# Kernel optimization log

Hardware: AMD Instinct MI355X
Metric: run time of the kernel (lower is better)

## Reference

```python
import jax, jax.numpy as jnp
import numpy as np

D_MODEL = 1024
N_HEADS = 16
HEAD_DIM = D_MODEL // N_HEADS
D_FF = 4096
LN_EPS = 1e-5


def _layernorm(x, g, b):
    mu = jnp.mean(x, axis=-1, keepdims=True)
    var = jnp.var(x, axis=-1, keepdims=True)
    return (x - mu) * jax.lax.rsqrt(var + LN_EPS) * g + b


def setup_inputs() -> dict:
    key = jax.random.key(0)
    ks = jax.random.split(key, 10)
    s = 0.02
    return {
        "hidden_states": jax.random.normal(ks[0], (2, 2048, D_MODEL), dtype=jnp.float32),
        "qkv_w": jax.random.normal(ks[1], (3 * D_MODEL, D_MODEL), dtype=jnp.float32) * s,
        "qkv_b": jnp.zeros((3 * D_MODEL,), dtype=jnp.float32),
        "out_w": jax.random.normal(ks[2], (D_MODEL, D_MODEL), dtype=jnp.float32) * s,
        "out_b": jnp.zeros((D_MODEL,), dtype=jnp.float32),
        "fc1_w": jax.random.normal(ks[3], (D_FF, D_MODEL), dtype=jnp.float32) * s,
        "fc1_b": jnp.zeros((D_FF,), dtype=jnp.float32),
        "fc2_w": jax.random.normal(ks[4], (D_MODEL, D_FF), dtype=jnp.float32) * s,
        "fc2_b": jnp.zeros((D_MODEL,), dtype=jnp.float32),
        "ln1_g": jnp.ones((D_MODEL,), dtype=jnp.float32),
        "ln1_b": jnp.zeros((D_MODEL,), dtype=jnp.float32),
        "ln2_g": jnp.ones((D_MODEL,), dtype=jnp.float32),
        "ln2_b": jnp.zeros((D_MODEL,), dtype=jnp.float32),
    }


def reference(hidden_states, qkv_w, qkv_b, out_w, out_b, fc1_w, fc1_b, fc2_w, fc2_b, ln1_g, ln1_b, ln2_g, ln2_b):
    B, S, D = hidden_states.shape
    scale = 1.0 / np.sqrt(HEAD_DIM).astype(np.float32)

    normed = _layernorm(hidden_states, ln1_g, ln1_b)
    qkv = normed @ qkv_w.T + qkv_b  # [B,S,3D]
    qkv = qkv.reshape(B, S, 3, N_HEADS, HEAD_DIM).transpose(2, 0, 3, 1, 4)
    q, k, v = qkv[0], qkv[1], qkv[2]  # [B,H,S,hd]

    scores = jnp.einsum("bhqd,bhkd->bhqk", q, k) * scale
    causal = jnp.tril(jnp.ones((S, S), dtype=bool))
    scores = jnp.where(causal, scores, jnp.float32(-jnp.inf))
    probs = jax.nn.softmax(scores, axis=-1)
    attn = jnp.einsum("bhqk,bhkd->bhqd", probs, v)  # [B,H,S,hd]
    attn = attn.transpose(0, 2, 1, 3).reshape(B, S, D)
    attn = attn @ out_w.T + out_b

    hidden = hidden_states + attn
    normed2 = _layernorm(hidden, ln2_g, ln2_b)
    ff = jax.nn.gelu(normed2 @ fc1_w.T + fc1_b, approximate=False)
    ff = ff @ fc2_w.T + fc2_b
    return hidden + ff
```

## Files before the change

### kernel.cpp

```cpp
#include <hip/hip_runtime.h>
#include <math.h>

using bf16   = __bf16;
using bf16x8 = __attribute__((ext_vector_type(8))) __bf16;
using bf16x4 = __attribute__((ext_vector_type(4))) __bf16;
using f32x4  = __attribute__((ext_vector_type(4))) float;
using f32x16 = __attribute__((ext_vector_type(16))) float;
using uint2v = __attribute__((ext_vector_type(2))) unsigned int;

#define MFMA_16x16x32(a, b, c) __builtin_amdgcn_mfma_f32_16x16x32_bf16((a), (b), (c), 0, 0, 0)
#define MFMA32(a, b, c) __builtin_amdgcn_mfma_f32_32x32x16_bf16((a), (b), (c), 0, 0, 0)

__device__ __forceinline__ void gll16(const void* g, void* l) {
  __builtin_amdgcn_global_load_lds((const __attribute__((address_space(1))) void*)g,
                                   (__attribute__((address_space(3))) void*)l,
                                   16, 0, 0);
}

__device__ __forceinline__ int cvtpk(float lo, float hi) {
  int r;
  asm("v_cvt_pk_bf16_f32 %0, %1, %2" : "=v"(r) : "v"(lo), "v"(hi));
  return r;
}

__device__ __forceinline__ float gelu_fast(float x) {
  const float u = 0.7978845608f * __builtin_fmaf(0.044715f * x, x * x, x);
  const float e = exp2f(2.885390082f * u);
  return x * e / (e + 1.f);
}

__global__ __launch_bounds__(256) void prep_kernel(const float* __restrict__ s0, bf16* d0,
                                                   const float* __restrict__ s1, bf16* d1,
                                                   const float* __restrict__ s2, bf16* d2,
                                                   const float* __restrict__ s3, bf16* d3,
                                                   const float* __restrict__ x,
                                                   const float* __restrict__ g,
                                                   const float* __restrict__ b,
                                                   bf16* __restrict__ lnout) {
  const int bid = blockIdx.x, t = threadIdx.x;
  if (bid < 12288) {
    int i = bid * 256 + t;
    const float* s;
    bf16* d;
    if (i < 786432) { s = s0; d = d0; }
    else if (i < 1048576) { s = s1; d = d1; i -= 786432; }
    else if (i < 2097152) { s = s2; d = d2; i -= 1048576; }
    else { s = s3; d = d3; i -= 2097152; }
    float4 v = ((const float4*)s)[i];
    bf16x4 o;
    o[0] = (bf16)v.x; o[1] = (bf16)v.y; o[2] = (bf16)v.z; o[3] = (bf16)v.w;
    ((bf16x4*)d)[i] = o;
    return;
  }
  const int row = bid - 12288;
  const float4 v = ((const float4*)(x + (size_t)row * 1024))[t];
  float s1v = v.x + v.y + v.z + v.w;
  float s2v = v.x * v.x + v.y * v.y + v.z * v.z + v.w * v.w;
#pragma unroll
  for (int d = 32; d; d >>= 1) {
    s1v += __shfl_xor(s1v, d);
    s2v += __shfl_xor(s2v, d);
  }
  __shared__ float red[8];
  const int w = t >> 6;
  if ((t & 63) == 0) { red[w] = s1v; red[4 + w] = s2v; }
  __syncthreads();
  s1v = red[0] + red[1] + red[2] + red[3];
  s2v = red[4] + red[5] + red[6] + red[7];
  const float mu = s1v * (1.f / 1024.f);
  const float rstd = rsqrtf(s2v * (1.f / 1024.f) - mu * mu + 1e-5f);
  const float4 gv = ((const float4*)g)[t];
  const float4 bv = ((const float4*)b)[t];
  bf16x4 o;
  o[0] = (bf16)((v.x - mu) * rstd * gv.x + bv.x);
  o[1] = (bf16)((v.y - mu) * rstd * gv.y + bv.y);
  o[2] = (bf16)((v.z - mu) * rstd * gv.z + bv.z);
  o[3] = (bf16)((v.w - mu) * rstd * gv.w + bv.w);
  ((bf16x4*)(lnout + (size_t)row * 1024))[t] = o;
}

__global__ __launch_bounds__(256) void ln_kernel(const bf16* __restrict__ x,
                                                 const float* __restrict__ g,
                                                 const float* __restrict__ b,
                                                 bf16* __restrict__ out) {
  const int row = blockIdx.x, t = threadIdx.x;
  const bf16x4 raw = ((const bf16x4*)(x + (size_t)row * 1024))[t];
  float4 v;
  v.x = (float)raw[0]; v.y = (float)raw[1]; v.z = (float)raw[2]; v.w = (float)raw[3];
  float s1 = v.x + v.y + v.z + v.w;
  float s2 = v.x * v.x + v.y * v.y + v.z * v.z + v.w * v.w;
#pragma unroll
  for (int d = 32; d; d >>= 1) {
    s1 += __shfl_xor(s1, d);
    s2 += __shfl_xor(s2, d);
  }
  __shared__ float red[8];
  const int w = t >> 6;
  if ((t & 63) == 0) { red[w] = s1; red[4 + w] = s2; }
  __syncthreads();
  s1 = red[0] + red[1] + red[2] + red[3];
  s2 = red[4] + red[5] + red[6] + red[7];
  const float mu = s1 * (1.f / 1024.f);
  const float rstd = rsqrtf(s2 * (1.f / 1024.f) - mu * mu + 1e-5f);
  const float4 gv = ((const float4*)g)[t];
  const float4 bv = ((const float4*)b)[t];
  bf16x4 o;
  o[0] = (bf16)((v.x - mu) * rstd * gv.x + bv.x);
  o[1] = (bf16)((v.y - mu) * rstd * gv.y + bv.y);
  o[2] = (bf16)((v.z - mu) * rstd * gv.z + bv.z);
  o[3] = (bf16)((v.w - mu) * rstd * gv.w + bv.w);
  ((bf16x4*)(out + (size_t)row * 1024))[t] = o;
}

template <int EPI>
__global__ __launch_bounds__(512, 2) void gemm256(const bf16* __restrict__ A,
                                                  const bf16* __restrict__ W,
                                                  const float* __restrict__ bias,
                                                  bf16* __restrict__ outp,
                                                  bf16* __restrict__ vout, int N, int K,
                                                  int nbx) {
  __shared__ __align__(1024) bf16 lds[65536];
  const int t = threadIdx.x, lane = t & 63, w = t >> 6;
  const int wm = w >> 2, wn = w & 3;
  const int l15 = lane & 15, lg = lane >> 4;

  const int nwg = gridDim.x, cpx = nwg >> 3, bid = blockIdx.x;
  const int swz = (bid & 7) * cpx + (bid >> 3);
  const int bx = swz % nbx, by = swz / nbx;
  const int m0 = by * 256, n0 = bx * 256;

  const bf16* src[8];
  int dst[8];
  {
    const int ss[2] = {t, t + 512};
#pragma unroll
    for (int i = 0; i < 2; i++) {
      const int d = ss[i] * 16;
      const int L = d ^ (((d >> 9) & 1) << 5);
      const int r = L >> 7, coff = (L & 127) >> 1;
#pragma unroll
      for (int hf = 0; hf < 2; hf++) {
        src[hf * 2 + i]     = A + (size_t)(m0 + hf * 128 + r) * K + coff;
        src[4 + hf * 2 + i] = W + (size_t)(n0 + hf * 128 + r) * K + coff;
        dst[hf * 2 + i]     = hf * 8192 + ss[i] * 8;
        dst[4 + hf * 2 + i] = 16384 + hf * 8192 + ss[i] * 8;
      }
    }
  }

#define STAGE256(db_)                                   \
  do {                                                  \
    _Pragma("unroll") for (int u = 0; u < 8; u++) {     \
      gll16(src[u], lds + (db_)*32768 + dst[u]);        \
      src[u] += 64;                                     \
    }                                                   \
  } while (0)

  f32x4 acc[8][4];
#pragma unroll
  for (int mi = 0; mi < 8; mi++)
#pragma unroll
    for (int ni = 0; ni < 4; ni++) acc[mi][ni] = (f32x4){0.f, 0.f, 0.f, 0.f};

  const int ntiles = K >> 6;
  STAGE256(0);
  asm volatile("s_waitcnt vmcnt(0)" ::: "memory");
  __builtin_amdgcn_s_barrier();

  for (int kt = 0; kt < ntiles; ++kt) {
    const int db = kt & 1;
    const bf16* Ab = lds + db * 32768 + wm * 8192;
    const bf16* Bb = lds + db * 32768 + 16384 + (wn >> 1) * 8192;
    bf16x8 bfr[4][2];
#pragma unroll
    for (int p = 0; p < 4; ++p) {
      bf16x8 af[2][2];
#pragma unroll
      for (int mi2 = 0; mi2 < 2; ++mi2)
#pragma unroll
        for (int ks = 0; ks < 2; ++ks) {
          const int row = (2 * p + mi2) * 16 + l15;
          const int Pb = (row * 128 + ks * 64 + lg * 16) ^ (((row >> 2) & 1) << 5);
          af[mi2][ks] = *(const bf16x8*)((const char*)Ab + Pb);
        }
      if (p == 0) {
#pragma unroll
        for (int ni = 0; ni < 4; ++ni)
#pragma unroll
          for (int ks = 0; ks < 2; ++ks) {
            const int row = (wn & 1) * 64 + ni * 16 + l15;
            const int Pb = (row * 128 + ks * 64 + lg * 16) ^ (((row >> 2) & 1) << 5);
            bfr[ni][ks] = *(const bf16x8*)((const char*)Bb + Pb);
          }
        if (kt + 1 < ntiles) STAGE256(db ^ 1);
      }
      __builtin_amdgcn_s_barrier();
      asm volatile("s_waitcnt lgkmcnt(0)" ::: "memory");
      __builtin_amdgcn_sched_barrier(0);
      __builtin_amdgcn_s_setprio(1);
#pragma unroll
      for (int ks = 0; ks < 2; ++ks)
#pragma unroll
        for (int ni = 0; ni < 4; ++ni) {
          acc[2 * p][ni] = MFMA_16x16x32(af[0][ks], bfr[ni][ks], acc[2 * p][ni]);
          acc[2 * p + 1][ni] = MFMA_16x16x32(af[1][ks], bfr[ni][ks], acc[2 * p + 1][ni]);
        }
      __builtin_amdgcn_s_setprio(0);
      if (p == 3) asm volatile("s_waitcnt vmcnt(0)" ::: "memory");
      __builtin_amdgcn_s_barrier();
    }
  }
#undef STAGE256

  const float csq = 0.18033688011112042f;
#pragma unroll
  for (int mi = 0; mi < 8; ++mi) {
    const int row0 = m0 + wm * 128 + mi * 16 + lg * 4;
#pragma unroll
    for (int ni = 0; ni < 4; ++ni) {
      const int col = n0 + wn * 64 + ni * 16 + l15;
      const float bc = bias[col];
      if (EPI == 0 && col >= 2048) {
        bf16x4 ov;
#pragma unroll
        for (int r = 0; r < 4; ++r) ov[r] = (bf16)(acc[mi][ni][r] + bc);
        const int bb = row0 >> 11, s = row0 & 2047, dc = col - 2048;
        *(bf16x4*)(vout + ((size_t)(bb * 16 + (dc >> 6)) * 64 + (dc & 63)) * 2048 + s) = ov;
      } else {
        float sc = 1.f;
        if (EPI == 0 && col < 1024) sc = csq;
#pragma unroll
        for (int r = 0; r < 4; ++r) {
          float v = acc[mi][ni][r] + bc;
          if (EPI == 1) v = gelu_fast(v);
          outp[(size_t)(row0 + r) * N + col] = (bf16)(v * sc);
        }
      }
    }
  }
}

template <int MODE>
__global__ __launch_bounds__(256, 3) void gemm64(const bf16* __restrict__ A,
                                                 const bf16* __restrict__ W,
                                                 const float* __restrict__ bias,
                                                 const void* __restrict__ residv,
                                                 void* __restrict__ outv, int N, int K,
                                                 int nbx) {
  __shared__ __align__(1024) bf16 lds[24576];
  const int t = threadIdx.x, lane = t & 63, w = t >> 6;
  const int wm = w >> 1, wn = w & 1;
  const int l15 = lane & 15, lg = lane >> 4;

  const int nwg = gridDim.x, cpx = nwg >> 3, bid = blockIdx.x;
  const int swz = (bid & 7) * cpx + (bid >> 3);
  const int bx = swz % nbx, by = swz / nbx;
  const int m0 = by * 64, n0 = bx * 128;

  const bf16* src[6];
  int dst[6];
#pragma unroll
  for (int u = 0; u < 2; ++u) {
    const int off = u * 4096 + t * 16;
    const int row = off >> 7, slot = (off >> 4) & 7;
    const int col = (slot ^ (row & 7)) * 8;
    src[u] = A + (size_t)(m0 + row) * K + col;
    dst[u] = off >> 1;
  }
#pragma unroll
  for (int u = 0; u < 4; ++u) {
    const int off = u * 4096 + t * 16;
    const int row = off >> 7, slot = (off >> 4) & 7;
    const int col = (slot ^ (row & 7)) * 8;
    src[2 + u] = W + (size_t)(n0 + row) * K + col;
    dst[2 + u] = 4096 + (off >> 1);
  }

#define STAGE64(db_)                                    \
  do {                                                  \
    _Pragma("unroll") for (int u = 0; u < 6; u++) {     \
      gll16(src[u], lds + (db_)*12288 + dst[u]);        \
      src[u] += 64;                                     \
    }                                                   \
  } while (0)

  f32x4 acc[2][4];
#pragma unroll
  for (int mi = 0; mi < 2; mi++)
#pragma unroll
    for (int ni = 0; ni < 4; ni++) acc[mi][ni] = (f32x4){0.f, 0.f, 0.f, 0.f};

  const int ntiles = K >> 6;
  STAGE64(0);
  asm volatile("s_waitcnt vmcnt(0)" ::: "memory");
  __builtin_amdgcn_s_barrier();

  for (int kt = 0; kt < ntiles; ++kt) {
    const int db = kt & 1;
    const char* Ab = (const char*)(lds + db * 12288);
    const char* Bb = (const char*)(lds + db * 12288 + 4096);
#pragma unroll
    for (int p = 0; p < 2; ++p) {
      bf16x8 af[2], bfr[4];
#pragma unroll
      for (int mi = 0; mi < 2; ++mi) {
        const int row = wm * 32 + mi * 16 + l15;
        af[mi] = *(const bf16x8*)(Ab + row * 128 + (((p * 4 + lg) ^ (row & 7)) << 4));
      }
#pragma unroll
      for (int ni = 0; ni < 4; ++ni) {
        const int row = wn * 64 + ni * 16 + l15;
        bfr[ni] = *(const bf16x8*)(Bb + row * 128 + (((p * 4 + lg) ^ (row & 7)) << 4));
      }
      if (p == 0 && kt + 1 < ntiles) STAGE64(db ^ 1);
      __builtin_amdgcn_s_barrier();
      asm volatile("s_waitcnt lgkmcnt(0)" ::: "memory");
      __builtin_amdgcn_sched_barrier(0);
      __builtin_amdgcn_s_setprio(1);
#pragma unroll
      for (int mi = 0; mi < 2; ++mi)
#pragma unroll
        for (int ni = 0; ni < 4; ++ni)
          acc[mi][ni] = MFMA_16x16x32(af[mi], bfr[ni], acc[mi][ni]);
      __builtin_amdgcn_s_setprio(0);
      if (p == 1) asm volatile("s_waitcnt vmcnt(0)" ::: "memory");
      __builtin_amdgcn_s_barrier();
    }
  }
#undef STAGE64

#pragma unroll
  for (int mi = 0; mi < 2; ++mi) {
    const int row0 = m0 + wm * 32 + mi * 16 + lg * 4;
#pragma unroll
    for (int ni = 0; ni < 4; ++ni) {
      const int col = n0 + wn * 64 + ni * 16 + l15;
      const float bc = bias[col];
#pragma unroll
      for (int r = 0; r < 4; ++r) {
        const size_t idx = (size_t)(row0 + r) * N + col;
        float v = acc[mi][ni][r] + bc;
        if (MODE == 0) {
          v += ((const float*)residv)[idx];
          ((bf16*)outv)[idx] = (bf16)v;
        } else {
          v += (float)((const bf16*)residv)[idx];
          ((float*)outv)[idx] = v;
        }
      }
    }
  }
}

__global__ __launch_bounds__(256) void attn_kernel(const bf16* __restrict__ qkv,
                                                   const bf16* __restrict__ vt,
                                                   bf16* __restrict__ attn_out) {
  __shared__ bf16 Ks[3][4096];
  __shared__ bf16 Vs[3][4096];
  const int t = threadIdx.x, lane = t & 63, w = t >> 6;
  const int l31 = lane & 31, lh = lane >> 5;
  const int bx = blockIdx.x, by = blockIdx.y;
  const int b = by >> 4, h = by & 15;
  const int g = (bx + by) & 15;
  const int qb = (by < 16) ? g : 15 - g;
  const int qw = qb * 128 + w * 32;
  const int qq = qw + l31;
  const int nt = 2 * qb + 2;

  bf16x8 qf[4];
  {
    const bf16* qp = qkv + (size_t)(b * 2048 + qq) * 3072 + h * 64 + lh * 8;
#pragma unroll
    for (int c = 0; c < 4; ++c) qf[c] = *(const bf16x8*)(qp + c * 16);
  }

  const int r0 = t >> 3, c16 = t & 7;
  const int swsl = 8 * (c16 ^ (r0 & 7));
  const bf16* kp0 = qkv + (size_t)(b * 2048 + r0) * 3072 + 1024 + h * 64 + swsl;
  const bf16* kp1 = qkv + (size_t)(b * 2048 + r0 + 32) * 3072 + 1024 + h * 64 + swsl;
  const bf16* vp0 = vt + ((size_t)by * 64 + r0) * 2048 + swsl;
  const bf16* vp1 = vp0 + (size_t)32 * 2048;

#define ASTAGE(buf)                          \
  do {                                       \
    gll16(kp0, &Ks[buf][t * 8]);             \
    gll16(kp1, &Ks[buf][2048 + t * 8]);      \
    gll16(vp0, &Vs[buf][t * 8]);             \
    gll16(vp1, &Vs[buf][2048 + t * 8]);      \
    kp0 += (size_t)64 * 3072;                \
    kp1 += (size_t)64 * 3072;                \
    vp0 += 64;                               \
    vp1 += 64;                               \
  } while (0)

  const f32x16 z16 = {0.f, 0.f, 0.f, 0.f, 0.f, 0.f, 0.f, 0.f,
                      0.f, 0.f, 0.f, 0.f, 0.f, 0.f, 0.f, 0.f};
  f32x16 o0a = z16, o0b = z16, o1a = z16, o1b = z16;
  float lsum = 0.f;

  ASTAGE(0);
  ASTAGE(1);
  int b0 = 0, b1 = 1, b2 = 2;
  for (int tt = 0; tt < nt; ++tt) {
    const int kv0 = tt * 64;
    if (tt < nt - 1) asm volatile("s_waitcnt vmcnt(4)" ::: "memory");
    else             asm volatile("s_waitcnt vmcnt(0)" ::: "memory");
    __builtin_amdgcn_s_barrier();
    if (tt + 2 < nt) ASTAGE(b2);
    if (kv0 <= qw + 31) {
      const bf16* kbp = Ks[b0];
      const bf16* vbp = Vs[b0];
      const bool up = (kv0 + 32) <= (qw + 31);
      f32x16 s0v = z16, s1v = z16;
      __builtin_amdgcn_s_setprio(1);
#pragma unroll
      for (int c = 0; c < 4; ++c) {
        const int slot = ((c * 2 + lh) ^ (l31 & 7)) * 16;
        const bf16x8 a0 = *(const bf16x8*)((const char*)kbp + l31 * 128 + slot);
        s0v = MFMA32(a0, qf[c], s0v);
      }
      if (up) {
#pragma unroll
        for (int c = 0; c < 4; ++c) {
          const int slot = ((c * 2 + lh) ^ (l31 & 7)) * 16;
          const bf16x8 a1 = *(const bf16x8*)((const char*)kbp + (32 + l31) * 128 + slot);
          s1v = MFMA32(a1, qf[c], s1v);
        }
      }
      __builtin_amdgcn_s_setprio(0);
      if (kv0 + 64 > qw) {
#pragma unroll
        for (int j = 0; j < 16; ++j) {
          const int kr = kv0 + (j & 3) + 8 * (j >> 2) + 4 * lh;
          if (kr > qq) s0v[j] = -1e30f;
          if (kr + 32 > qq) s1v[j] = -1e30f;
        }
      }
#pragma unroll
      for (int j = 0; j < 16; ++j) {
        s0v[j] = exp2f(s0v[j]);
        lsum += s0v[j];
      }
      if (up) {
#pragma unroll
        for (int j = 0; j < 16; ++j) {
          s1v[j] = exp2f(s1v[j]);
          lsum += s1v[j];
        }
      }
      unsigned int w0[8];
#pragma unroll
      for (int j = 0; j < 8; ++j) w0[j] = (unsigned int)cvtpk(s0v[2 * j], s0v[2 * j + 1]);
#define PVHALF2(WW, KB, OA, OB)                                                      \
  do {                                                                               \
    const uint2v e0 = __builtin_amdgcn_permlane32_swap(WW[0], WW[2], false, false);  \
    const uint2v e1 = __builtin_amdgcn_permlane32_swap(WW[1], WW[3], false, false);  \
    const uint2v e2 = __builtin_amdgcn_permlane32_swap(WW[4], WW[6], false, false);  \
    const uint2v e3 = __builtin_amdgcn_permlane32_swap(WW[5], WW[7], false, false);  \
    union { unsigned int i[4]; bf16x8 v; } pA, pB;                                   \
    pA.i[0] = e0[0]; pA.i[1] = e1[0]; pA.i[2] = e0[1]; pA.i[3] = e1[1];              \
    pB.i[0] = e2[0]; pB.i[1] = e3[0]; pB.i[2] = e2[1]; pB.i[3] = e3[1];              \
    const int sA = (((KB)*4 + lh) ^ (l31 & 7)) * 16;                                 \
    const int sB = (((KB)*4 + 2 + lh) ^ (l31 & 7)) * 16;                             \
    const bf16x8 vA0 = *(const bf16x8*)((const char*)vbp + l31 * 128 + sA);          \
    const bf16x8 vA1 = *(const bf16x8*)((const char*)vbp + (32 + l31) * 128 + sA);   \
    const bf16x8 vB0 = *(const bf16x8*)((const char*)vbp + l31 * 128 + sB);          \
    const bf16x8 vB1 = *(const bf16x8*)((const char*)vbp + (32 + l31) * 128 + sB);   \
    OA = MFMA32(vA0, pA.v, OA);                                                      \
    OB = MFMA32(vA1, pA.v, OB);                                                      \
    OA = MFMA32(vB0, pB.v, OA);                                                      \
    OB = MFMA32(vB1, pB.v, OB);                                                      \
  } while (0)
      __builtin_amdgcn_s_setprio(1);
      PVHALF2(w0, 0, o0a, o1a);
      __builtin_amdgcn_s_setprio(0);
      if (up) {
        unsigned int w1[8];
#pragma unroll
        for (int j = 0; j < 8; ++j) w1[j] = (unsigned int)cvtpk(s1v[2 * j], s1v[2 * j + 1]);
        __builtin_amdgcn_s_setprio(1);
        PVHALF2(w1, 1, o0b, o1b);
        __builtin_amdgcn_s_setprio(0);
      }
#undef PVHALF2
    }
    const int tmp = b0; b0 = b1; b1 = b2; b2 = tmp;
  }
#undef ASTAGE

  lsum += __shfl_xor(lsum, 32);
  const float rinv = 1.f / lsum;
  const f32x16 oacc0 = o0a + o0b, oacc1 = o1a + o1b;
  bf16* op = attn_out + (size_t)(b * 2048 + qq) * 1024 + h * 64;
#pragma unroll
  for (int gR = 0; gR < 4; ++gR) {
    bf16x4 o0, o1;
#pragma unroll
    for (int r = 0; r < 4; ++r) {
      o0[r] = (bf16)(oacc0[4 * gR + r] * rinv);
      o1[r] = (bf16)(oacc1[4 * gR + r] * rinv);
    }
    *(bf16x4*)(op + 8 * gR + 4 * lh) = o0;
    *(bf16x4*)(op + 32 + 8 * gR + 4 * lh) = o1;
  }
}

extern "C" void kernel_launch(void* const* d_in, const int* in_sizes, int n_in,
                              void* d_out, int out_size, void* d_ws, size_t ws_size,
                              hipStream_t stream) {
  (void)in_sizes; (void)n_in; (void)out_size; (void)ws_size;
  const float* hidden = (const float*)d_in[0];
  const float* qkv_w  = (const float*)d_in[1];
  const float* qkv_b  = (const float*)d_in[2];
  const float* out_w  = (const float*)d_in[3];
  const float* out_b  = (const float*)d_in[4];
  const float* fc1_w  = (const float*)d_in[5];
  const float* fc1_b  = (const float*)d_in[6];
  const float* fc2_w  = (const float*)d_in[7];
  const float* fc2_b  = (const float*)d_in[8];
  const float* ln1_g  = (const float*)d_in[9];
  const float* ln1_b  = (const float*)d_in[10];
  const float* ln2_g  = (const float*)d_in[11];
  const float* ln2_b  = (const float*)d_in[12];
  float* outp = (float*)d_out;

  char* ws = (char*)d_ws;
  bf16*  ln1o  = (bf16*)(ws);
  bf16*  qkvb  = (bf16*)(ws + ((size_t)8 << 20));
  bf16*  vtb   = (bf16*)(ws + ((size_t)32 << 20));
  bf16*  atto  = (bf16*)(ws + ((size_t)40 << 20));
  bf16*  res1b = (bf16*)(ws + ((size_t)48 << 20));
  bf16*  ln2o  = (bf16*)(ws + ((size_t)64 << 20));
  bf16*  ff1   = (bf16*)(ws + ((size_t)72 << 20));
  bf16*  wqkv  = (bf16*)(ws + ((size_t)104 << 20));
  bf16*  wout  = (bf16*)(ws + ((size_t)110 << 20));
  bf16*  wfc1  = (bf16*)(ws + ((size_t)112 << 20));
  bf16*  wfc2  = (bf16*)(ws + ((size_t)120 << 20));

  prep_kernel<<<16384, 256, 0, stream>>>(qkv_w, wqkv, out_w, wout, fc1_w, wfc1, fc2_w, wfc2,
                                         hidden, ln1_g, ln1_b, ln1o);
  gemm256<0><<<192, 512, 0, stream>>>(ln1o, wqkv, qkv_b, qkvb, vtb, 3072, 1024, 12);
  attn_kernel<<<dim3(16, 32), 256, 0, stream>>>(qkvb, vtb, atto);
  gemm64<0><<<512, 256, 0, stream>>>(atto, wout, out_b, hidden, res1b, 1024, 1024, 8);
  ln_kernel<<<4096, 256, 0, stream>>>(res1b, ln2_g, ln2_b, ln2o);
  gemm256<1><<<256, 512, 0, stream>>>(ln2o, wfc1, fc1_b, ff1, nullptr, 4096, 1024, 16);
  gemm64<1><<<512, 256, 0, stream>>>(ff1, wfc2, fc2_b, res1b, outp, 1024, 4096, 8);
}
```

Baseline: 229.4 us.

## Overlap out/fc1/fc2 weight bf16 conversion with attention kernel via extra blocks

Moves the fp32-to-bf16 conversion of the out-projection, fc1 and fc2 weights out of the prep kernel and into extra blocks appended to the attention grid. The prep kernel now only converts the QKV weight and does LayerNorm. This lets the memory-bound conversion fill idle CUs while the attention kernel's compute-bound, causally imbalanced blocks run. The risk is that the conversion blocks compete with attention blocks for bandwidth and scheduling slots, and the attention kernel may lengthen.

Result: slower. 241.0 us (+5.0%).

```diff
diff --git a/kernel.cpp b/kernel.cpp
--- a/kernel.cpp
+++ b/kernel.cpp
@@ -30,29 +30,20 @@
 }
 
 __global__ __launch_bounds__(256) void prep_kernel(const float* __restrict__ s0, bf16* d0,
-                                                   const float* __restrict__ s1, bf16* d1,
-                                                   const float* __restrict__ s2, bf16* d2,
-                                                   const float* __restrict__ s3, bf16* d3,
                                                    const float* __restrict__ x,
                                                    const float* __restrict__ g,
                                                    const float* __restrict__ b,
                                                    bf16* __restrict__ lnout) {
   const int bid = blockIdx.x, t = threadIdx.x;
-  if (bid < 12288) {
-    int i = bid * 256 + t;
-    const float* s;
-    bf16* d;
-    if (i < 786432) { s = s0; d = d0; }
-    else if (i < 1048576) { s = s1; d = d1; i -= 786432; }
-    else if (i < 2097152) { s = s2; d = d2; i -= 1048576; }
-    else { s = s3; d = d3; i -= 2097152; }
-    float4 v = ((const float4*)s)[i];
+  if (bid < 3072) {
+    const int i = bid * 256 + t;
+    float4 v = ((const float4*)s0)[i];
     bf16x4 o;
     o[0] = (bf16)v.x; o[1] = (bf16)v.y; o[2] = (bf16)v.z; o[3] = (bf16)v.w;
-    ((bf16x4*)d)[i] = o;
+    ((bf16x4*)d0)[i] = o;
     return;
   }
-  const int row = bid - 12288;
+  const int row = bid - 3072;
   const float4 v = ((const float4*)(x + (size_t)row * 1024))[t];
   float s1v = v.x + v.y + v.z + v.w;
   float s2v = v.x * v.x + v.y * v.y + v.z * v.z + v.w * v.w;
@@ -354,12 +345,34 @@
 
 __global__ __launch_bounds__(256) void attn_kernel(const bf16* __restrict__ qkv,
                                                    const bf16* __restrict__ vt,
-                                                   bf16* __restrict__ attn_out) {
+                                                   bf16* __restrict__ attn_out,
+                                                   const float* __restrict__ cw0, bf16* cd0,
+                                                   const float* __restrict__ cw1, bf16* cd1,
+                                                   const float* __restrict__ cw2, bf16* cd2) {
   __shared__ bf16 Ks[3][4096];
   __shared__ bf16 Vs[3][4096];
   const int t = threadIdx.x, lane = t & 63, w = t >> 6;
   const int l31 = lane & 31, lh = lane >> 5;
   const int bx = blockIdx.x, by = blockIdx.y;
+
+  if (bx >= 16) {
+    int i = ((bx - 16) * 32 + by) * 9216 + t;
+#pragma unroll 4
+    for (int it = 0; it < 36; ++it, i += 256) {
+      const float* s;
+      bf16* d;
+      int j = i;
+      if (j < 262144) { s = cw0; d = cd0; }
+      else if (j < 1310720) { s = cw1; d = cd1; j -= 262144; }
+      else { s = cw2; d = cd2; j -= 1310720; }
+      float4 v = ((const float4*)s)[j];
+      bf16x4 o;
+      o[0] = (bf16)v.x; o[1] = (bf16)v.y; o[2] = (bf16)v.z; o[3] = (bf16)v.w;
+      ((bf16x4*)d)[j] = o;
+    }
+    return;
+  }
+
   const int b = by >> 4, h = by & 15;
   const int g = (bx + by) & 15;
   const int qb = (by < 16) ? g : 15 - g;
@@ -537,10 +550,10 @@
   bf16*  wfc1  = (bf16*)(ws + ((size_t)112 << 20));
   bf16*  wfc2  = (bf16*)(ws + ((size_t)120 << 20));
 
-  prep_kernel<<<16384, 256, 0, stream>>>(qkv_w, wqkv, out_w, wout, fc1_w, wfc1, fc2_w, wfc2,
-                                         hidden, ln1_g, ln1_b, ln1o);
+  prep_kernel<<<7168, 256, 0, stream>>>(qkv_w, wqkv, hidden, ln1_g, ln1_b, ln1o);
   gemm256<0><<<192, 512, 0, stream>>>(ln1o, wqkv, qkv_b, qkvb, vtb, 3072, 1024, 12);
-  attn_kernel<<<dim3(16, 32), 256, 0, stream>>>(qkvb, vtb, atto);
+  attn_kernel<<<dim3(24, 32), 256, 0, stream>>>(qkvb, vtb, atto,
+                                                out_w, wout, fc1_w, wfc1, fc2_w, wfc2);
   gemm64<0><<<512, 256, 0, stream>>>(atto, wout, out_b, hidden, res1b, 1024, 1024, 8);
   ln_kernel<<<4096, 256, 0, stream>>>(res1b, ln2_g, ln2_b, ln2o);
   gemm256<1><<<256, 512, 0, stream>>>(ln2o, wfc1, fc1_b, ff1, nullptr, 4096, 1024, 16);
```

## Split attention KV range across two blocks and merge partials in a combine kernel

Applied to the files above, without the earlier changes.

Each causal query block's KV tiles are now split into two halves handled by separate workgroups, doubling the attention grid and shortening each block's serial KV loop. The partial unnormalized outputs and row sums are written in fp32 to workspace, and a new combine kernel sums them, normalizes and writes bf16. This is meant to improve load balance and occupancy across compute units. In exchange it adds a large fp32 write and read round trip plus an extra kernel launch. The merge relies on both halves sharing the same softmax reference, so it needs no max rescaling.

Measured after the change: 242.0 us. 1.05x slower.

```diff
diff --git a/kernel.cpp b/kernel.cpp
--- a/kernel.cpp
+++ b/kernel.cpp
@@ -354,18 +354,20 @@
 
 __global__ __launch_bounds__(256) void attn_kernel(const bf16* __restrict__ qkv,
                                                    const bf16* __restrict__ vt,
-                                                   bf16* __restrict__ attn_out) {
+                                                   float* __restrict__ pO,
+                                                   float* __restrict__ pls) {
   __shared__ bf16 Ks[3][4096];
   __shared__ bf16 Vs[3][4096];
   const int t = threadIdx.x, lane = t & 63, w = t >> 6;
   const int l31 = lane & 31, lh = lane >> 5;
   const int bx = blockIdx.x, by = blockIdx.y;
   const int b = by >> 4, h = by & 15;
-  const int g = (bx + by) & 15;
-  const int qb = (by < 16) ? g : 15 - g;
+  const int gg = (bx + by) & 31;
+  const int qb = gg >> 1, sx = gg & 1;
   const int qw = qb * 128 + w * 32;
   const int qq = qw + l31;
-  const int nt = 2 * qb + 2;
+  const int nt = qb + 1;
+  const int t0 = sx * nt;
 
   bf16x8 qf[4];
   {
@@ -376,9 +378,9 @@
 
   const int r0 = t >> 3, c16 = t & 7;
   const int swsl = 8 * (c16 ^ (r0 & 7));
-  const bf16* kp0 = qkv + (size_t)(b * 2048 + r0) * 3072 + 1024 + h * 64 + swsl;
-  const bf16* kp1 = qkv + (size_t)(b * 2048 + r0 + 32) * 3072 + 1024 + h * 64 + swsl;
-  const bf16* vp0 = vt + ((size_t)by * 64 + r0) * 2048 + swsl;
+  const bf16* kp0 = qkv + (size_t)(b * 2048 + t0 * 64 + r0) * 3072 + 1024 + h * 64 + swsl;
+  const bf16* kp1 = kp0 + (size_t)32 * 3072;
+  const bf16* vp0 = vt + ((size_t)by * 64 + r0) * 2048 + t0 * 64 + swsl;
   const bf16* vp1 = vp0 + (size_t)32 * 2048;
 
 #define ASTAGE(buf)                          \
@@ -402,7 +404,7 @@
   ASTAGE(1);
   int b0 = 0, b1 = 1, b2 = 2;
   for (int tt = 0; tt < nt; ++tt) {
-    const int kv0 = tt * 64;
+    const int kv0 = (t0 + tt) * 64;
     if (tt < nt - 1) asm volatile("s_waitcnt vmcnt(4)" ::: "memory");
     else             asm volatile("s_waitcnt vmcnt(0)" ::: "memory");
     __builtin_amdgcn_s_barrier();
@@ -489,20 +491,38 @@
 #undef ASTAGE
 
   lsum += __shfl_xor(lsum, 32);
-  const float rinv = 1.f / lsum;
+  if (lh == 0) pls[sx * 65536 + by * 2048 + qq] = lsum;
   const f32x16 oacc0 = o0a + o0b, oacc1 = o1a + o1b;
-  bf16* op = attn_out + (size_t)(b * 2048 + qq) * 1024 + h * 64;
+  float* pop = pO + (size_t)sx * 4194304 + (size_t)(b * 2048 + qq) * 1024 + h * 64;
 #pragma unroll
   for (int gR = 0; gR < 4; ++gR) {
-    bf16x4 o0, o1;
+    f32x4 q0, q1;
 #pragma unroll
     for (int r = 0; r < 4; ++r) {
-      o0[r] = (bf16)(oacc0[4 * gR + r] * rinv);
-      o1[r] = (bf16)(oacc1[4 * gR + r] * rinv);
-    }
-    *(bf16x4*)(op + 8 * gR + 4 * lh) = o0;
-    *(bf16x4*)(op + 32 + 8 * gR + 4 * lh) = o1;
-  }
+      q0[r] = oacc0[4 * gR + r];
+      q1[r] = oacc1[4 * gR + r];
+    }
+    *(f32x4*)(pop + 8 * gR + 4 * lh) = q0;
+    *(f32x4*)(pop + 32 + 8 * gR + 4 * lh) = q1;
+  }
+}
+
+__global__ __launch_bounds__(256) void attn_combine(const float* __restrict__ pO,
+                                                    const float* __restrict__ pls,
+                                                    bf16* __restrict__ atto) {
+  const int row = blockIdx.x;
+  const int t = threadIdx.x;
+  const int col = t * 4;
+  const int b = row >> 11, s = row & 2047, h = col >> 6;
+  const int lsidx = (b * 16 + h) * 2048 + s;
+  const float rinv = 1.f / (pls[lsidx] + pls[65536 + lsidx]);
+  const size_t io = (size_t)row * 1024 + col;
+  const f32x4 a = *(const f32x4*)(pO + io);
+  const f32x4 c = *(const f32x4*)(pO + 4194304 + io);
+  bf16x4 o;
+#pragma unroll
+  for (int r = 0; r < 4; ++r) o[r] = (bf16)((a[r] + c[r]) * rinv);
+  *(bf16x4*)(atto + io) = o;
 }
 
 extern "C" void kernel_launch(void* const* d_in, const int* in_sizes, int n_in,
@@ -532,6 +552,8 @@
   bf16*  res1b = (bf16*)(ws + ((size_t)48 << 20));
   bf16*  ln2o  = (bf16*)(ws + ((size_t)64 << 20));
   bf16*  ff1   = (bf16*)(ws + ((size_t)72 << 20));
+  float* pO    = (float*)(ws + ((size_t)48 << 20));
+  float* plsb  = (float*)(ws + ((size_t)80 << 20));
   bf16*  wqkv  = (bf16*)(ws + ((size_t)104 << 20));
   bf16*  wout  = (bf16*)(ws + ((size_t)110 << 20));
   bf16*  wfc1  = (bf16*)(ws + ((size_t)112 << 20));
@@ -540,7 +562,8 @@
   prep_kernel<<<16384, 256, 0, stream>>>(qkv_w, wqkv, out_w, wout, fc1_w, wfc1, fc2_w, wfc2,
                                          hidden, ln1_g, ln1_b, ln1o);
   gemm256<0><<<192, 512, 0, stream>>>(ln1o, wqkv, qkv_b, qkvb, vtb, 3072, 1024, 12);
-  attn_kernel<<<dim3(16, 32), 256, 0, stream>>>(qkvb, vtb, atto);
+  attn_kernel<<<dim3(32, 32), 256, 0, stream>>>(qkvb, vtb, pO, plsb);
+  attn_combine<<<4096, 256, 0, stream>>>(pO, plsb, atto);
   gemm64<0><<<512, 256, 0, stream>>>(atto, wout, out_b, hidden, res1b, 1024, 1024, 8);
   ln_kernel<<<4096, 256, 0, stream>>>(res1b, ln2_g, ln2_b, ln2o);
   gemm256<1><<<256, 512, 0, stream>>>(ln2o, wfc1, fc1_b, ff1, nullptr, 4096, 1024, 16);
```
